# Optimization experiments

Hardware: AMD Instinct MI355X
Metric: run time of the kernel (lower is better)

Reference implementation:

```python
import jax, jax.numpy as jnp
import numpy as np

B, N, D = 32, 1024, 512

def setup_inputs() -> dict:
    key = jax.random.key(0)
    ks = jax.random.split(key, 5)
    s = 1.0 / np.sqrt(D)
    return {
        "x": jax.random.normal(ks[0], (B, N, D), jnp.float32),
        "Wq": jax.random.normal(ks[1], (D, D), jnp.float32) * s,
        "bq": jnp.zeros((D,), jnp.float32),
        "Wk": jax.random.normal(ks[2], (D, D), jnp.float32) * s,
        "bk": jnp.zeros((D,), jnp.float32),
        "Wv": jax.random.normal(ks[3], (D, D), jnp.float32) * s,
        "bv": jnp.zeros((D,), jnp.float32),
        "pos_bias": jax.random.normal(ks[4], (N, N), jnp.float32) * 0.02,
    }

def reference(x, Wq, bq, Wk, bk, Wv, bv, pos_bias):
    # torch nn.Linear: y = x @ W.T + b
    q = x @ Wq.T + bq                      # [B,N,D]
    k = x @ Wk.T + bk                      # [B,N,D]
    v = x @ Wv.T + bv                      # [B,N,D]
    # AFT-full: out[b,t,d] = sig(q)[b,t,d] * sum_s exp(k[b,s,d]+w[t,s]) v[b,s,d]
    #                                        / sum_s exp(k[b,s,d]+w[t,s])
    # exp(k+w) factors as exp(w)*exp(k); the num/den ratio is invariant to
    # per-row shifts of w and per-(b,d) shifts of k, so stabilize both.
    w = pos_bias - jnp.max(pos_bias, axis=1, keepdims=True)   # [T,S]
    kk = k - jnp.max(k, axis=1, keepdims=True)                # [B,S,D]
    ew = jnp.exp(w)
    ek = jnp.exp(kk)
    num = jnp.einsum('ts,bsd->btd', ew, ek * v)               # [B,T,D]
    den = jnp.einsum('ts,bsd->btd', ew, ek)                   # [B,T,D]
    return jax.nn.sigmoid(q) * (num / den)
```

## Files before the change

kernel.cpp:

```cpp
#include <hip/hip_runtime.h>

typedef unsigned short u16;
typedef unsigned int u32;
using frag8 = __attribute__((ext_vector_type(8))) short;
using f32x4 = __attribute__((ext_vector_type(4))) float;

__device__ __forceinline__ u16 f2bf(float f) {
  union { float f; u32 u; } x;
  x.f = f;
  u32 r = (x.u + 0x7fffu + ((x.u >> 16) & 1u)) >> 16;
  return (u16)r;
}

__device__ __forceinline__ void stage_tile64(const u16* g, int ld, u16* lds, int tid) {
  const int wv = tid >> 6;
#pragma unroll
  for (int i = 0; i < 4; ++i) {
    const int c = i * 256 + tid;
    const int row = c >> 3;
    const int colc = (c & 7) ^ (row & 7);
    __builtin_amdgcn_global_load_lds(
        (const __attribute__((address_space(1))) void*)(g + (size_t)row * ld + colc * 8),
        (__attribute__((address_space(3))) void*)(lds + (size_t)(i * 256 + wv * 64) * 8),
        16, 0, 0);
  }
}

__device__ __forceinline__ frag8 frag_read64(const u16* lds, int row, int kk, int quad) {
  const int cc = (kk * 4 + quad) ^ (row & 7);
  return *(const frag8*)&lds[row * 64 + cc * 8];
}

__global__ void prep_kernel(const float* __restrict__ x, const float* __restrict__ Wq,
                            const float* __restrict__ Wk, const float* __restrict__ Wv,
                            const float* __restrict__ pb, u16* __restrict__ xb,
                            u16* __restrict__ wqb, u16* __restrict__ wkb,
                            u16* __restrict__ wvb, u16* __restrict__ ewb) {
  const int blk = blockIdx.x;
  const float* src;
  u16* dst;
  int base;
  bool ex = false;
  if (blk < 16384)      { src = x;  dst = xb;  base = blk; }
  else if (blk < 16640) { src = Wq; dst = wqb; base = blk - 16384; }
  else if (blk < 16896) { src = Wk; dst = wkb; base = blk - 16640; }
  else if (blk < 17152) { src = Wv; dst = wvb; base = blk - 16896; }
  else                  { src = pb; dst = ewb; base = blk - 17152; ex = true; }
  const int i = base * 256 + threadIdx.x;
  float4 v = ((const float4*)src)[i];
  ushort4 o;
  if (ex) {
    o.x = f2bf(__expf(v.x)); o.y = f2bf(__expf(v.y));
    o.z = f2bf(__expf(v.z)); o.w = f2bf(__expf(v.w));
  } else {
    o.x = f2bf(v.x); o.y = f2bf(v.y); o.z = f2bf(v.z); o.w = f2bf(v.w);
  }
  ((ushort4*)dst)[i] = o;
}

__global__ __launch_bounds__(256, 3) void q_kernel(const u16* __restrict__ xb,
                                                   const u16* __restrict__ wqb,
                                                   const float* __restrict__ bq,
                                                   float* __restrict__ out) {
  __shared__ __align__(16) u16 As[128 * 64];
  __shared__ __align__(16) u16 Bs[128 * 64];
  const int tid = threadIdx.x;
  const int lane = tid & 63, wv = tid >> 6;
  const int wm = (wv & 1) * 64, wn = (wv >> 1) * 64;
  const int fr = lane & 15, quad = lane >> 4;
  const int m0 = blockIdx.y * 128;
  const int n0 = blockIdx.x * 128;
  f32x4 acc[4][4] = {};
  for (int k0 = 0; k0 < 512; k0 += 64) {
    stage_tile64(xb + (size_t)m0 * 512 + k0, 512, As, tid);
    stage_tile64(wqb + (size_t)n0 * 512 + k0, 512, Bs, tid);
    __syncthreads();
#pragma unroll
    for (int kk = 0; kk < 2; ++kk) {
      frag8 a[4], b[4];
#pragma unroll
      for (int i = 0; i < 4; ++i) {
        a[i] = frag_read64(As, wm + i * 16 + fr, kk, quad);
        b[i] = frag_read64(Bs, wn + i * 16 + fr, kk, quad);
      }
#pragma unroll
      for (int mi = 0; mi < 4; ++mi)
#pragma unroll
        for (int ni = 0; ni < 4; ++ni)
          acc[mi][ni] = __builtin_amdgcn_mfma_f32_16x16x32_bf16(a[mi], b[ni], acc[mi][ni], 0, 0, 0);
    }
    __syncthreads();
  }
#pragma unroll
  for (int mi = 0; mi < 4; ++mi)
#pragma unroll
    for (int ni = 0; ni < 4; ++ni) {
      const int col = n0 + wn + ni * 16 + fr;
      const float bqv = bq[col];
#pragma unroll
      for (int r = 0; r < 4; ++r) {
        const int row = m0 + wm + mi * 16 + quad * 4 + r;
        const float qv = acc[mi][ni][r] + bqv;
        out[(size_t)row * 512 + col] = 1.0f / (1.0f + __expf(-qv));
      }
    }
}

__global__ __launch_bounds__(256, 2) void kv_kernel(const u16* __restrict__ xb,
                                                    const u16* __restrict__ wkb,
                                                    const u16* __restrict__ wvb,
                                                    const float* __restrict__ bk,
                                                    const float* __restrict__ bv,
                                                    u16* __restrict__ ekT,
                                                    u16* __restrict__ ekvT) {
  __shared__ __align__(16) u16 Ak[128 * 64];
  __shared__ __align__(16) u16 Av[128 * 64];
  __shared__ __align__(16) u16 Bs[128 * 64];
  const int tid = threadIdx.x;
  const int lane = tid & 63, wv = tid >> 6;
  const int wm = (wv & 1) * 64, wn = (wv >> 1) * 64;
  const int fr = lane & 15, quad = lane >> 4;
  const int s0 = blockIdx.x * 128;
  const int d0 = blockIdx.y * 128;
  const int b  = blockIdx.z;
  f32x4 acck[4][4] = {}, accv[4][4] = {};
  for (int k0 = 0; k0 < 512; k0 += 64) {
    stage_tile64(wkb + (size_t)d0 * 512 + k0, 512, Ak, tid);
    stage_tile64(wvb + (size_t)d0 * 512 + k0, 512, Av, tid);
    stage_tile64(xb + ((size_t)b * 1024 + s0) * 512 + k0, 512, Bs, tid);
    __syncthreads();
#pragma unroll
    for (int kk = 0; kk < 2; ++kk) {
      frag8 ak[4], av[4], bb[4];
#pragma unroll
      for (int i = 0; i < 4; ++i) {
        ak[i] = frag_read64(Ak, wm + i * 16 + fr, kk, quad);
        av[i] = frag_read64(Av, wm + i * 16 + fr, kk, quad);
        bb[i] = frag_read64(Bs, wn + i * 16 + fr, kk, quad);
      }
#pragma unroll
      for (int mi = 0; mi < 4; ++mi)
#pragma unroll
        for (int ni = 0; ni < 4; ++ni) {
          acck[mi][ni] = __builtin_amdgcn_mfma_f32_16x16x32_bf16(ak[mi], bb[ni], acck[mi][ni], 0, 0, 0);
          accv[mi][ni] = __builtin_amdgcn_mfma_f32_16x16x32_bf16(av[mi], bb[ni], accv[mi][ni], 0, 0, 0);
        }
    }
    __syncthreads();
  }
#pragma unroll
  for (int mi = 0; mi < 4; ++mi)
#pragma unroll
    for (int r = 0; r < 4; ++r) {
      const int d = d0 + wm + mi * 16 + quad * 4 + r;
      const float bkv = bk[d], bvv = bv[d];
#pragma unroll
      for (int ni = 0; ni < 4; ++ni) {
        const int s = s0 + wn + ni * 16 + fr;
        const float ek = __expf(acck[mi][ni][r] + bkv);
        const float vv = accv[mi][ni][r] + bvv;
        const size_t idx = ((size_t)b * 512 + d) * 1024 + s;
        ekT[idx]  = f2bf(ek);
        ekvT[idx] = f2bf(ek * vv);
      }
    }
}

__global__ __launch_bounds__(256, 2) void aft_kernel(const u16* __restrict__ ew,
                                                     const u16* __restrict__ ekT,
                                                     const u16* __restrict__ ekvT,
                                                     float* __restrict__ out) {
  __shared__ __align__(16) u16 As[128 * 64];
  __shared__ __align__(16) u16 B1[128 * 64];
  __shared__ __align__(16) u16 B2[128 * 64];
  const int tid = threadIdx.x;
  const int lane = tid & 63, wv = tid >> 6;
  const int wm = (wv & 1) * 64, wn = (wv >> 1) * 64;
  const int fr = lane & 15, quad = lane >> 4;
  const int d0 = blockIdx.x * 128;
  const int t0 = blockIdx.y * 128;
  const int b  = blockIdx.z;
  f32x4 accn[4][4] = {}, accd[4][4] = {};
  for (int k0 = 0; k0 < 1024; k0 += 64) {
    stage_tile64(ew + (size_t)t0 * 1024 + k0, 1024, As, tid);
    stage_tile64(ekvT + ((size_t)b * 512 + d0) * 1024 + k0, 1024, B1, tid);
    stage_tile64(ekT + ((size_t)b * 512 + d0) * 1024 + k0, 1024, B2, tid);
    __syncthreads();
#pragma unroll
    for (int kk = 0; kk < 2; ++kk) {
      frag8 a[4], b1[4], b2[4];
#pragma unroll
      for (int i = 0; i < 4; ++i) {
        a[i]  = frag_read64(As, wm + i * 16 + fr, kk, quad);
        b1[i] = frag_read64(B1, wn + i * 16 + fr, kk, quad);
        b2[i] = frag_read64(B2, wn + i * 16 + fr, kk, quad);
      }
#pragma unroll
      for (int mi = 0; mi < 4; ++mi)
#pragma unroll
        for (int ni = 0; ni < 4; ++ni) {
          accn[mi][ni] = __builtin_amdgcn_mfma_f32_16x16x32_bf16(a[mi], b1[ni], accn[mi][ni], 0, 0, 0);
          accd[mi][ni] = __builtin_amdgcn_mfma_f32_16x16x32_bf16(a[mi], b2[ni], accd[mi][ni], 0, 0, 0);
        }
    }
    __syncthreads();
  }
#pragma unroll
  for (int mi = 0; mi < 4; ++mi)
#pragma unroll
    for (int ni = 0; ni < 4; ++ni)
#pragma unroll
      for (int r = 0; r < 4; ++r) {
        const int t = t0 + wm + mi * 16 + quad * 4 + r;
        const int d = d0 + wn + ni * 16 + fr;
        const size_t idx = ((size_t)b * 1024 + t) * 512 + d;
        const float sq = out[idx];
        out[idx] = sq * accn[mi][ni][r] / accd[mi][ni][r];
      }
}

extern "C" void kernel_launch(void* const* d_in, const int* in_sizes, int n_in,
                              void* d_out, int out_size, void* d_ws, size_t ws_size,
                              hipStream_t stream) {
  const float* x  = (const float*)d_in[0];
  const float* Wq = (const float*)d_in[1];
  const float* bq = (const float*)d_in[2];
  const float* Wk = (const float*)d_in[3];
  const float* bk = (const float*)d_in[4];
  const float* Wv = (const float*)d_in[5];
  const float* bv = (const float*)d_in[6];
  const float* pb = (const float*)d_in[7];
  float* out = (float*)d_out;
  char* ws = (char*)d_ws;
  u16* xb   = (u16*)(ws);
  u16* wqb  = (u16*)(ws + 33554432);
  u16* wkb  = (u16*)(ws + 34078720);
  u16* wvb  = (u16*)(ws + 34603008);
  u16* ewb  = (u16*)(ws + 35127296);
  u16* ekT  = (u16*)(ws + 37224448);
  u16* ekvT = (u16*)(ws + 70778880);

  prep_kernel<<<18176, 256, 0, stream>>>(x, Wq, Wk, Wv, pb, xb, wqb, wkb, wvb, ewb);
  q_kernel<<<dim3(4, 256), 256, 0, stream>>>(xb, wqb, bq, out);
  kv_kernel<<<dim3(8, 4, 32), 256, 0, stream>>>(xb, wkb, wvb, bk, bv, ekT, ekvT);
  aft_kernel<<<dim3(4, 8, 32), 256, 0, stream>>>(ewb, ekT, ekvT, out);
}
```

Measured before the change: 256.9 us.

## Double-buffer AFT GEMM with interleaved async loads and larger 256-row tiles

Rewrites the AFT mixing kernel to use 512 threads per block with a 256-row time tile, so each staged ek/ekv tile is reused across twice as many rows. LDS is double-buffered: loads for the next k-slice are issued in chunks between MFMA phases, with explicit vmcnt/lgkmcnt waits, raw barriers and setprio, to overlap global-to-LDS traffic with matrix math. It uses 128KB of LDS per block and has complex manual synchronisation, which limits occupancy and risks races if the wait counts are wrong.

```diff
diff --git a/kernel.cpp b/kernel.cpp
--- a/kernel.cpp
+++ b/kernel.cpp
@@ -24,6 +24,16 @@
         (__attribute__((address_space(3))) void*)(lds + (size_t)(i * 256 + wv * 64) * 8),
         16, 0, 0);
   }
+}
+
+__device__ __forceinline__ void stage64(const u16* g, u16* l, int tid) {
+  const int wv = tid >> 6;
+  const int row = tid >> 3;
+  const int colc = (tid & 7) ^ (row & 7);
+  __builtin_amdgcn_global_load_lds(
+      (const __attribute__((address_space(1))) void*)(g + (size_t)row * 1024 + (size_t)colc * 8),
+      (__attribute__((address_space(3))) void*)(l + (size_t)wv * 512),
+      16, 0, 0);
 }
 
 __device__ __forceinline__ frag8 frag_read64(const u16* lds, int row, int kk, int quad) {
@@ -166,34 +176,132 @@
     }
 }
 
-__global__ __launch_bounds__(256, 2) void aft_kernel(const u16* __restrict__ ew,
+#define AFT_BUF (512 * 64)
+__global__ __launch_bounds__(512, 2) void aft_kernel(const u16* __restrict__ ew,
                                                      const u16* __restrict__ ekT,
                                                      const u16* __restrict__ ekvT,
                                                      float* __restrict__ out) {
-  __shared__ __align__(16) u16 As[128 * 64];
-  __shared__ __align__(16) u16 B1[128 * 64];
-  __shared__ __align__(16) u16 B2[128 * 64];
+  __shared__ __align__(16) u16 lds[2 * AFT_BUF];
   const int tid = threadIdx.x;
   const int lane = tid & 63, wv = tid >> 6;
-  const int wm = (wv & 1) * 64, wn = (wv >> 1) * 64;
+  const int wm = (wv >> 1) * 64;
+  const int wn = (wv & 1) * 64;
   const int fr = lane & 15, quad = lane >> 4;
   const int d0 = blockIdx.x * 128;
-  const int t0 = blockIdx.y * 128;
+  const int t0 = blockIdx.y * 256;
   const int b  = blockIdx.z;
+
+  const u16* Ag  = ew + (size_t)t0 * 1024;
+  const u16* B1g = ekvT + ((size_t)b * 512 + d0) * 1024;
+  const u16* B2g = ekT  + ((size_t)b * 512 + d0) * 1024;
+
   f32x4 accn[4][4] = {}, accd[4][4] = {};
-  for (int k0 = 0; k0 < 1024; k0 += 64) {
-    stage_tile64(ew + (size_t)t0 * 1024 + k0, 1024, As, tid);
-    stage_tile64(ekvT + ((size_t)b * 512 + d0) * 1024 + k0, 1024, B1, tid);
-    stage_tile64(ekT + ((size_t)b * 512 + d0) * 1024 + k0, 1024, B2, tid);
-    __syncthreads();
+
+#pragma unroll
+  for (int i = 0; i < 4; ++i)
+    stage64(Ag + (size_t)i * 64 * 1024, lds + i * 4096, tid);
+#pragma unroll
+  for (int i = 0; i < 2; ++i)
+    stage64(B1g + (size_t)i * 64 * 1024, lds + 16384 + i * 4096, tid);
+#pragma unroll
+  for (int i = 0; i < 2; ++i)
+    stage64(B2g + (size_t)i * 64 * 1024, lds + 24576 + i * 4096, tid);
+  asm volatile("s_waitcnt vmcnt(0)" ::: "memory");
+  __builtin_amdgcn_s_barrier();
+
+  int cur = 0;
+  for (int k = 0; k < 15; ++k) {
+    u16* C  = lds + cur * AFT_BUF;
+    u16* Nx = lds + (cur ^ 1) * AFT_BUF;
+    const u16* An  = Ag  + (size_t)(k + 1) * 64;
+    const u16* B1n = B1g + (size_t)(k + 1) * 64;
+    const u16* B2n = B2g + (size_t)(k + 1) * 64;
+    frag8 a[4], bb[4];
+
+    stage64(An,                     Nx,        tid);
+    stage64(An + (size_t)64 * 1024, Nx + 4096, tid);
+#pragma unroll
+    for (int i = 0; i < 4; ++i) a[i]  = frag_read64(C,         wm + i * 16 + fr, 0, quad);
+#pragma unroll
+    for (int i = 0; i < 4; ++i) bb[i] = frag_read64(C + 16384, wn + i * 16 + fr, 0, quad);
+    __builtin_amdgcn_s_barrier();
+    asm volatile("s_waitcnt lgkmcnt(0)" ::: "memory");
+    __builtin_amdgcn_sched_barrier(0);
+    __builtin_amdgcn_s_setprio(1);
+#pragma unroll
+    for (int mi = 0; mi < 4; ++mi)
+#pragma unroll
+      for (int ni = 0; ni < 4; ++ni)
+        accn[mi][ni] = __builtin_amdgcn_mfma_f32_16x16x32_bf16(a[mi], bb[ni], accn[mi][ni], 0, 0, 0);
+    __builtin_amdgcn_s_setprio(0);
+    asm volatile("s_waitcnt vmcnt(2)" ::: "memory");
+    __builtin_amdgcn_s_barrier();
+
+    stage64(An + (size_t)128 * 1024, Nx + 8192,  tid);
+    stage64(An + (size_t)192 * 1024, Nx + 12288, tid);
+#pragma unroll
+    for (int i = 0; i < 4; ++i) bb[i] = frag_read64(C + 24576, wn + i * 16 + fr, 0, quad);
+    __builtin_amdgcn_s_barrier();
+    asm volatile("s_waitcnt lgkmcnt(0)" ::: "memory");
+    __builtin_amdgcn_sched_barrier(0);
+    __builtin_amdgcn_s_setprio(1);
+#pragma unroll
+    for (int mi = 0; mi < 4; ++mi)
+#pragma unroll
+      for (int ni = 0; ni < 4; ++ni)
+        accd[mi][ni] = __builtin_amdgcn_mfma_f32_16x16x32_bf16(a[mi], bb[ni], accd[mi][ni], 0, 0, 0);
+    __builtin_amdgcn_s_setprio(0);
+    __builtin_amdgcn_s_barrier();
+
+    stage64(B1n,                     Nx + 16384, tid);
+    stage64(B1n + (size_t)64 * 1024, Nx + 20480, tid);
+#pragma unroll
+    for (int i = 0; i < 4; ++i) a[i]  = frag_read64(C,         wm + i * 16 + fr, 1, quad);
+#pragma unroll
+    for (int i = 0; i < 4; ++i) bb[i] = frag_read64(C + 16384, wn + i * 16 + fr, 1, quad);
+    __builtin_amdgcn_s_barrier();
+    asm volatile("s_waitcnt lgkmcnt(0)" ::: "memory");
+    __builtin_amdgcn_sched_barrier(0);
+    __builtin_amdgcn_s_setprio(1);
+#pragma unroll
+    for (int mi = 0; mi < 4; ++mi)
+#pragma unroll
+      for (int ni = 0; ni < 4; ++ni)
+        accn[mi][ni] = __builtin_amdgcn_mfma_f32_16x16x32_bf16(a[mi], bb[ni], accn[mi][ni], 0, 0, 0);
+    __builtin_amdgcn_s_setprio(0);
+    __builtin_amdgcn_s_barrier();
+
+    stage64(B2n,                     Nx + 24576, tid);
+    stage64(B2n + (size_t)64 * 1024, Nx + 28672, tid);
+#pragma unroll
+    for (int i = 0; i < 4; ++i) bb[i] = frag_read64(C + 24576, wn + i * 16 + fr, 1, quad);
+    __builtin_amdgcn_s_barrier();
+    asm volatile("s_waitcnt lgkmcnt(0)" ::: "memory");
+    __builtin_amdgcn_sched_barrier(0);
+    __builtin_amdgcn_s_setprio(1);
+#pragma unroll
+    for (int mi = 0; mi < 4; ++mi)
+#pragma unroll
+      for (int ni = 0; ni < 4; ++ni)
+        accd[mi][ni] = __builtin_amdgcn_mfma_f32_16x16x32_bf16(a[mi], bb[ni], accd[mi][ni], 0, 0, 0);
+    __builtin_amdgcn_s_setprio(0);
+    asm volatile("s_waitcnt vmcnt(2)" ::: "memory");
+    __builtin_amdgcn_s_barrier();
+    cur ^= 1;
+  }
+
+  {
+    u16* C = lds + cur * AFT_BUF;
+    asm volatile("s_waitcnt vmcnt(0)" ::: "memory");
+    __builtin_amdgcn_s_barrier();
 #pragma unroll
     for (int kk = 0; kk < 2; ++kk) {
       frag8 a[4], b1[4], b2[4];
 #pragma unroll
       for (int i = 0; i < 4; ++i) {
-        a[i]  = frag_read64(As, wm + i * 16 + fr, kk, quad);
-        b1[i] = frag_read64(B1, wn + i * 16 + fr, kk, quad);
-        b2[i] = frag_read64(B2, wn + i * 16 + fr, kk, quad);
+        a[i]  = frag_read64(C,         wm + i * 16 + fr, kk, quad);
+        b1[i] = frag_read64(C + 16384, wn + i * 16 + fr, kk, quad);
+        b2[i] = frag_read64(C + 24576, wn + i * 16 + fr, kk, quad);
       }
 #pragma unroll
       for (int mi = 0; mi < 4; ++mi)
@@ -203,8 +311,8 @@
           accd[mi][ni] = __builtin_amdgcn_mfma_f32_16x16x32_bf16(a[mi], b2[ni], accd[mi][ni], 0, 0, 0);
         }
     }
-    __syncthreads();
-  }
+  }
+
 #pragma unroll
   for (int mi = 0; mi < 4; ++mi)
 #pragma unroll
@@ -243,5 +351,5 @@
   prep_kernel<<<18176, 256, 0, stream>>>(x, Wq, Wk, Wv, pb, xb, wqb, wkb, wvb, ewb);
   q_kernel<<<dim3(4, 256), 256, 0, stream>>>(xb, wqb, bq, out);
   kv_kernel<<<dim3(8, 4, 32), 256, 0, stream>>>(xb, wkb, wvb, bk, bv, ekT, ekvT);
-  aft_kernel<<<dim3(4, 8, 32), 256, 0, stream>>>(ewb, ekT, ekvT, out);
-}
+  aft_kernel<<<dim3(4, 4, 32), 512, 0, stream>>>(ewb, ekT, ekvT, out);
+}
```

Measured after the change: 251.7 us. -2.0%, faster.

## Merge Q and KV projection kernels into one interleaved launch; coarsen prep

Applied to the files above, without the earlier changes.

Combines the Q-projection and K/V-projection GEMM kernels into a single launch of 2048 blocks, where even blocks compute sigmoid(q) tiles and odd blocks compute exp(k) and exp(k)*v tiles. This cuts one launch and lets the lighter Q blocks fill gaps beside the heavier KV blocks. The prep kernel now has each block convert 4 float4 chunks, so it launches a quarter as many blocks. The fused kernel uses 48KB of LDS and launch bounds of 2 for both paths, which may lower occupancy for the Q path compared with its former bound of 3.

```diff
diff --git a/kernel.cpp b/kernel.cpp
--- a/kernel.cpp
+++ b/kernel.cpp
@@ -41,129 +41,133 @@
   u16* dst;
   int base;
   bool ex = false;
-  if (blk < 16384)      { src = x;  dst = xb;  base = blk; }
-  else if (blk < 16640) { src = Wq; dst = wqb; base = blk - 16384; }
-  else if (blk < 16896) { src = Wk; dst = wkb; base = blk - 16640; }
-  else if (blk < 17152) { src = Wv; dst = wvb; base = blk - 16896; }
-  else                  { src = pb; dst = ewb; base = blk - 17152; ex = true; }
-  const int i = base * 256 + threadIdx.x;
-  float4 v = ((const float4*)src)[i];
-  ushort4 o;
-  if (ex) {
-    o.x = f2bf(__expf(v.x)); o.y = f2bf(__expf(v.y));
-    o.z = f2bf(__expf(v.z)); o.w = f2bf(__expf(v.w));
-  } else {
-    o.x = f2bf(v.x); o.y = f2bf(v.y); o.z = f2bf(v.z); o.w = f2bf(v.w);
-  }
-  ((ushort4*)dst)[i] = o;
-}
-
-__global__ __launch_bounds__(256, 3) void q_kernel(const u16* __restrict__ xb,
-                                                   const u16* __restrict__ wqb,
-                                                   const float* __restrict__ bq,
-                                                   float* __restrict__ out) {
-  __shared__ __align__(16) u16 As[128 * 64];
-  __shared__ __align__(16) u16 Bs[128 * 64];
+  if (blk < 4096)      { src = x;  dst = xb;  base = blk; }
+  else if (blk < 4160) { src = Wq; dst = wqb; base = blk - 4096; }
+  else if (blk < 4224) { src = Wk; dst = wkb; base = blk - 4160; }
+  else if (blk < 4288) { src = Wv; dst = wvb; base = blk - 4224; }
+  else                 { src = pb; dst = ewb; base = blk - 4288; ex = true; }
+#pragma unroll
+  for (int j = 0; j < 4; ++j) {
+    const int i = base * 1024 + j * 256 + threadIdx.x;
+    float4 v = ((const float4*)src)[i];
+    ushort4 o;
+    if (ex) {
+      o.x = f2bf(__expf(v.x)); o.y = f2bf(__expf(v.y));
+      o.z = f2bf(__expf(v.z)); o.w = f2bf(__expf(v.w));
+    } else {
+      o.x = f2bf(v.x); o.y = f2bf(v.y); o.z = f2bf(v.z); o.w = f2bf(v.w);
+    }
+    ((ushort4*)dst)[i] = o;
+  }
+}
+
+__global__ __launch_bounds__(256, 2) void qkv_kernel(const u16* __restrict__ xb,
+                                                     const u16* __restrict__ wqb,
+                                                     const u16* __restrict__ wkb,
+                                                     const u16* __restrict__ wvb,
+                                                     const float* __restrict__ bq,
+                                                     const float* __restrict__ bk,
+                                                     const float* __restrict__ bv,
+                                                     float* __restrict__ out,
+                                                     u16* __restrict__ ekT,
+                                                     u16* __restrict__ ekvT) {
+  __shared__ __align__(16) u16 sh[3 * 128 * 64];
   const int tid = threadIdx.x;
   const int lane = tid & 63, wv = tid >> 6;
   const int wm = (wv & 1) * 64, wn = (wv >> 1) * 64;
   const int fr = lane & 15, quad = lane >> 4;
-  const int m0 = blockIdx.y * 128;
-  const int n0 = blockIdx.x * 128;
-  f32x4 acc[4][4] = {};
-  for (int k0 = 0; k0 < 512; k0 += 64) {
-    stage_tile64(xb + (size_t)m0 * 512 + k0, 512, As, tid);
-    stage_tile64(wqb + (size_t)n0 * 512 + k0, 512, Bs, tid);
-    __syncthreads();
-#pragma unroll
-    for (int kk = 0; kk < 2; ++kk) {
-      frag8 a[4], b[4];
-#pragma unroll
-      for (int i = 0; i < 4; ++i) {
-        a[i] = frag_read64(As, wm + i * 16 + fr, kk, quad);
-        b[i] = frag_read64(Bs, wn + i * 16 + fr, kk, quad);
-      }
-#pragma unroll
-      for (int mi = 0; mi < 4; ++mi)
-#pragma unroll
-        for (int ni = 0; ni < 4; ++ni)
-          acc[mi][ni] = __builtin_amdgcn_mfma_f32_16x16x32_bf16(a[mi], b[ni], acc[mi][ni], 0, 0, 0);
-    }
-    __syncthreads();
-  }
-#pragma unroll
-  for (int mi = 0; mi < 4; ++mi)
-#pragma unroll
-    for (int ni = 0; ni < 4; ++ni) {
-      const int col = n0 + wn + ni * 16 + fr;
-      const float bqv = bq[col];
+  const int bid = blockIdx.x;
+
+  if ((bid & 1) == 0) {
+    const int qb = bid >> 1;
+    const int n0 = (qb & 3) * 128;
+    const int m0 = (qb >> 2) * 128;
+    u16* As = sh;
+    u16* Bs = sh + 8192;
+    f32x4 acc[4][4] = {};
+    for (int k0 = 0; k0 < 512; k0 += 64) {
+      stage_tile64(xb + (size_t)m0 * 512 + k0, 512, As, tid);
+      stage_tile64(wqb + (size_t)n0 * 512 + k0, 512, Bs, tid);
+      __syncthreads();
+#pragma unroll
+      for (int kk = 0; kk < 2; ++kk) {
+        frag8 a[4], b[4];
+#pragma unroll
+        for (int i = 0; i < 4; ++i) {
+          a[i] = frag_read64(As, wm + i * 16 + fr, kk, quad);
+          b[i] = frag_read64(Bs, wn + i * 16 + fr, kk, quad);
+        }
+#pragma unroll
+        for (int mi = 0; mi < 4; ++mi)
+#pragma unroll
+          for (int ni = 0; ni < 4; ++ni)
+            acc[mi][ni] = __builtin_amdgcn_mfma_f32_16x16x32_bf16(a[mi], b[ni], acc[mi][ni], 0, 0, 0);
+      }
+      __syncthreads();
+    }
+#pragma unroll
+    for (int mi = 0; mi < 4; ++mi)
+#pragma unroll
+      for (int ni = 0; ni < 4; ++ni) {
+        const int col = n0 + wn + ni * 16 + fr;
+        const float bqv = bq[col];
+#pragma unroll
+        for (int r = 0; r < 4; ++r) {
+          const int row = m0 + wm + mi * 16 + quad * 4 + r;
+          const float qv = acc[mi][ni][r] + bqv;
+          out[(size_t)row * 512 + col] = 1.0f / (1.0f + __expf(-qv));
+        }
+      }
+  } else {
+    const int kvb = bid >> 1;
+    const int s0 = (kvb & 7) * 128;
+    const int d0 = ((kvb >> 3) & 3) * 128;
+    const int b  = kvb >> 5;
+    u16* Ak = sh;
+    u16* Av = sh + 8192;
+    u16* Bs = sh + 16384;
+    f32x4 acck[4][4] = {}, accv[4][4] = {};
+    for (int k0 = 0; k0 < 512; k0 += 64) {
+      stage_tile64(wkb + (size_t)d0 * 512 + k0, 512, Ak, tid);
+      stage_tile64(wvb + (size_t)d0 * 512 + k0, 512, Av, tid);
+      stage_tile64(xb + ((size_t)b * 1024 + s0) * 512 + k0, 512, Bs, tid);
+      __syncthreads();
+#pragma unroll
+      for (int kk = 0; kk < 2; ++kk) {
+        frag8 ak[4], av[4], bb[4];
+#pragma unroll
+        for (int i = 0; i < 4; ++i) {
+          ak[i] = frag_read64(Ak, wm + i * 16 + fr, kk, quad);
+          av[i] = frag_read64(Av, wm + i * 16 + fr, kk, quad);
+          bb[i] = frag_read64(Bs, wn + i * 16 + fr, kk, quad);
+        }
+#pragma unroll
+        for (int mi = 0; mi < 4; ++mi)
+#pragma unroll
+          for (int ni = 0; ni < 4; ++ni) {
+            acck[mi][ni] = __builtin_amdgcn_mfma_f32_16x16x32_bf16(ak[mi], bb[ni], acck[mi][ni], 0, 0, 0);
+            accv[mi][ni] = __builtin_amdgcn_mfma_f32_16x16x32_bf16(av[mi], bb[ni], accv[mi][ni], 0, 0, 0);
+          }
+      }
+      __syncthreads();
+    }
+#pragma unroll
+    for (int mi = 0; mi < 4; ++mi)
 #pragma unroll
       for (int r = 0; r < 4; ++r) {
-        const int row = m0 + wm + mi * 16 + quad * 4 + r;
-        const float qv = acc[mi][ni][r] + bqv;
-        out[(size_t)row * 512 + col] = 1.0f / (1.0f + __expf(-qv));
-      }
-    }
-}
-
-__global__ __launch_bounds__(256, 2) void kv_kernel(const u16* __restrict__ xb,
-                                                    const u16* __restrict__ wkb,
-                                                    const u16* __restrict__ wvb,
-                                                    const float* __restrict__ bk,
-                                                    const float* __restrict__ bv,
-                                                    u16* __restrict__ ekT,
-                                                    u16* __restrict__ ekvT) {
-  __shared__ __align__(16) u16 Ak[128 * 64];
-  __shared__ __align__(16) u16 Av[128 * 64];
-  __shared__ __align__(16) u16 Bs[128 * 64];
-  const int tid = threadIdx.x;
-  const int lane = tid & 63, wv = tid >> 6;
-  const int wm = (wv & 1) * 64, wn = (wv >> 1) * 64;
-  const int fr = lane & 15, quad = lane >> 4;
-  const int s0 = blockIdx.x * 128;
-  const int d0 = blockIdx.y * 128;
-  const int b  = blockIdx.z;
-  f32x4 acck[4][4] = {}, accv[4][4] = {};
-  for (int k0 = 0; k0 < 512; k0 += 64) {
-    stage_tile64(wkb + (size_t)d0 * 512 + k0, 512, Ak, tid);
-    stage_tile64(wvb + (size_t)d0 * 512 + k0, 512, Av, tid);
-    stage_tile64(xb + ((size_t)b * 1024 + s0) * 512 + k0, 512, Bs, tid);
-    __syncthreads();
-#pragma unroll
-    for (int kk = 0; kk < 2; ++kk) {
-      frag8 ak[4], av[4], bb[4];
-#pragma unroll
-      for (int i = 0; i < 4; ++i) {
-        ak[i] = frag_read64(Ak, wm + i * 16 + fr, kk, quad);
-        av[i] = frag_read64(Av, wm + i * 16 + fr, kk, quad);
-        bb[i] = frag_read64(Bs, wn + i * 16 + fr, kk, quad);
-      }
-#pragma unroll
-      for (int mi = 0; mi < 4; ++mi)
+        const int d = d0 + wm + mi * 16 + quad * 4 + r;
+        const float bkv = bk[d], bvv = bv[d];
 #pragma unroll
         for (int ni = 0; ni < 4; ++ni) {
-          acck[mi][ni] = __builtin_amdgcn_mfma_f32_16x16x32_bf16(ak[mi], bb[ni], acck[mi][ni], 0, 0, 0);
-          accv[mi][ni] = __builtin_amdgcn_mfma_f32_16x16x32_bf16(av[mi], bb[ni], accv[mi][ni], 0, 0, 0);
-        }
-    }
-    __syncthreads();
-  }
-#pragma unroll
-  for (int mi = 0; mi < 4; ++mi)
-#pragma unroll
-    for (int r = 0; r < 4; ++r) {
-      const int d = d0 + wm + mi * 16 + quad * 4 + r;
-      const float bkv = bk[d], bvv = bv[d];
-#pragma unroll
-      for (int ni = 0; ni < 4; ++ni) {
-        const int s = s0 + wn + ni * 16 + fr;
-        const float ek = __expf(acck[mi][ni][r] + bkv);
-        const float vv = accv[mi][ni][r] + bvv;
-        const size_t idx = ((size_t)b * 512 + d) * 1024 + s;
-        ekT[idx]  = f2bf(ek);
-        ekvT[idx] = f2bf(ek * vv);
-      }
-    }
+          const int s = s0 + wn + ni * 16 + fr;
+          const float ek = __expf(acck[mi][ni][r] + bkv);
+          const float vv = accv[mi][ni][r] + bvv;
+          const size_t idx = ((size_t)b * 512 + d) * 1024 + s;
+          ekT[idx]  = f2bf(ek);
+          ekvT[idx] = f2bf(ek * vv);
+        }
+      }
+  }
 }
 
 __global__ __launch_bounds__(256, 2) void aft_kernel(const u16* __restrict__ ew,
@@ -240,8 +244,7 @@
   u16* ekT  = (u16*)(ws + 37224448);
   u16* ekvT = (u16*)(ws + 70778880);
 
-  prep_kernel<<<18176, 256, 0, stream>>>(x, Wq, Wk, Wv, pb, xb, wqb, wkb, wvb, ewb);
-  q_kernel<<<dim3(4, 256), 256, 0, stream>>>(xb, wqb, bq, out);
-  kv_kernel<<<dim3(8, 4, 32), 256, 0, stream>>>(xb, wkb, wvb, bk, bv, ekT, ekvT);
+  prep_kernel<<<4544, 256, 0, stream>>>(x, Wq, Wk, Wv, pb, xb, wqb, wkb, wvb, ewb);
+  qkv_kernel<<<2048, 256, 0, stream>>>(xb, wqb, wkb, wvb, bq, bk, bv, out, ekT, ekvT);
   aft_kernel<<<dim3(4, 8, 32), 256, 0, stream>>>(ewb, ekT, ekvT, out);
 }
```

New measurement: 267.8 us. 1.04x slower.
